# Optimization experiments

Hardware: AMD Instinct MI355X
Metric: run time of the kernel (lower is better)

## Reference

```python
import jax, jax.numpy as jnp
import numpy as np


def setup_inputs() -> dict:
    key = jax.random.key(0)
    ks = jax.random.split(key, 16)
    B, D, H = 65536, 64, 512
    s = 0.05
    inp = {
        "state": jax.random.normal(ks[0], (B, D), dtype=jnp.float32),
        "Wz0": jax.random.normal(ks[1], (H, D), dtype=jnp.float32) * s,
        "bz0": jax.random.normal(ks[2], (H,), dtype=jnp.float32) * s,
        "Wz1": jax.random.normal(ks[3], (H, H), dtype=jnp.float32) * s,
        "Wz2": jax.random.normal(ks[4], (H, H), dtype=jnp.float32) * s,
        "Wz3": jax.random.normal(ks[5], (H, H), dtype=jnp.float32) * s,
        "WzL": jax.random.normal(ks[6], (1, H), dtype=jnp.float32) * s,
        "Wx0": jax.random.normal(ks[7], (H, D), dtype=jnp.float32) * s,
        "bx0": jax.random.normal(ks[8], (H,), dtype=jnp.float32) * s,
        "Wx1": jax.random.normal(ks[9], (H, D), dtype=jnp.float32) * s,
        "bx1": jax.random.normal(ks[10], (H,), dtype=jnp.float32) * s,
        "Wx2": jax.random.normal(ks[11], (H, D), dtype=jnp.float32) * s,
        "bx2": jax.random.normal(ks[12], (H,), dtype=jnp.float32) * s,
        "WxL": jax.random.normal(ks[13], (1, D), dtype=jnp.float32) * s,
    }
    return inp


def reference(state, Wz0, bz0, Wz1, Wz2, Wz3, WzL, Wx0, bx0, Wx1, bx1, Wx2, bx2, WxL):
    sp = jax.nn.softplus

    def icnn_sum(x):  # x: [B, D] -> scalar (sum of per-sample convex outputs)
        z = sp(x @ Wz0.T + bz0)                      # [B, H]
        z = sp(z @ Wz1.T + x @ Wx0.T + bx0)          # [B, H]
        z = sp(z @ Wz2.T + x @ Wx1.T + bx1)          # [B, H]
        z = sp(z @ Wz3.T + x @ Wx2.T + bx2)          # [B, H]
        out = z @ WzL.T + x @ WxL.T                  # [B, 1]
        return out.sum()

    x = state - 1.0
    # Output is scalar per-sample, so grad of the batch-sum equals the stacked
    # per-sample jacobians computed by the torch Python loop.
    action = jax.grad(icnn_sum)(x)                   # [B, D]
    return action
```

## Files before the change

kernel.cpp:

```cpp
#include <hip/hip_runtime.h>

typedef unsigned short u16;
typedef unsigned int u32;
typedef unsigned long long u64;

#define B_TOTAL 65536
#define H 512
#define D 64
#define BM 64

typedef __bf16 bf16x8 __attribute__((ext_vector_type(8)));
typedef float f32x4 __attribute__((ext_vector_type(4)));

__device__ __forceinline__ u32 f2b(float f) {
  u32 u = __builtin_bit_cast(u32, f);
  return (u + 0x7fffu + ((u >> 16) & 1u)) >> 16;
}
__device__ __forceinline__ u16 f2bc(float f) {
  return __builtin_bit_cast(u16, (__bf16)f);
}
__device__ __forceinline__ float b2f(u32 bits) {
  return __builtin_bit_cast(float, bits << 16);
}

#define OFF_Wz0b 0
#define OFF_Wx0b 32768
#define OFF_Wx1b 65536
#define OFF_Wx2b 98304
#define OFF_Wz1b 131072
#define OFF_Wz2b 393216
#define OFF_Wz3b 655360
#define OFF_Wz1t 917504
#define OFF_Wz2t 1179648
#define OFF_Wz3t 1441792
#define OFF_Wz0t 1703936
#define OFF_Wx0t 1736704
#define OFF_Wx1t 1769472
#define OFF_Wx2t 1802240
#define OFF_WEND 1835008
#define WS_ELEMS OFF_WEND

__global__ __launch_bounds__(256) void prep_kernel(
    const float* __restrict__ Wz0, const float* __restrict__ Wz1,
    const float* __restrict__ Wz2, const float* __restrict__ Wz3,
    const float* __restrict__ Wx0, const float* __restrict__ Wx1,
    const float* __restrict__ Wx2, u16* __restrict__ wsb) {
  int i = blockIdx.x * 256 + threadIdx.x;
  const float* src;
  int NN, KK, trans, p;
  if (i < 131072) {
    int r = i >> 15; p = i & 32767;
    src = (r == 0) ? Wz0 : (r == 1) ? Wx0 : (r == 2) ? Wx1 : Wx2;
    NN = 512; KK = 64; trans = 0;
  } else if (i < 917504) {
    int j = i - 131072; int r = j >> 18; p = j & 262143;
    src = (r == 0) ? Wz1 : (r == 1) ? Wz2 : Wz3;
    NN = 512; KK = 512; trans = 0;
  } else if (i < 1703936) {
    int j = i - 917504; int r = j >> 18; p = j & 262143;
    src = (r == 0) ? Wz1 : (r == 1) ? Wz2 : Wz3;
    NN = 512; KK = 512; trans = 1;
  } else {
    int j = i - 1703936; int r = j >> 15; p = j & 32767;
    src = (r == 0) ? Wz0 : (r == 1) ? Wx0 : (r == 2) ? Wx1 : Wx2;
    NN = 64; KK = 512; trans = 1;
  }
  int jj = p & 7, lane = (p >> 3) & 63, blk = p >> 9;
  int kt_sh = (KK == 64) ? 1 : 4;
  int ntile = blk >> kt_sh;
  int kstep = blk & ((1 << kt_sh) - 1);
  int n = ntile * 16 + (lane & 15);
  int k = kstep * 32 + ((lane >> 4) << 3) + jj;
  float v = trans ? src[k * NN + n] : src[n * KK + k];
  wsb[i] = (u16)f2b(v);
}

__global__ __launch_bounds__(256) void fill_sentinel(float* out, int n) {
  int i = blockIdx.x * 256 + threadIdx.x;
  if (i < n) out[i] = 12345.0f;
}

__global__ __launch_bounds__(1024, 4) void icnn_kernel(
    const float* __restrict__ state,
    const float* __restrict__ bz0, const float* __restrict__ bx0,
    const float* __restrict__ bx1, const float* __restrict__ bx2,
    const float* __restrict__ WzL, const float* __restrict__ WxL,
    u16* __restrict__ wsw, float* __restrict__ out) {
  __shared__ u16 zbA[BM * H];
  __shared__ u16 zbB[BM * H];
  __shared__ u16 xbuf[BM * 72];

  const int tid = threadIdx.x;
  const int w = tid >> 6;
  const int lane = tid & 63;
  const int l15 = lane & 15;
  const int q = lane >> 4;
  const int blk = blockIdx.x;

  const u16* Wz0b = wsw + OFF_Wz0b;
  const u16* Wx0b = wsw + OFF_Wx0b;
  const u16* Wx1b = wsw + OFF_Wx1b;
  const u16* Wx2b = wsw + OFF_Wx2b;
  const u16* Wz1b = wsw + OFF_Wz1b;
  const u16* Wz2b = wsw + OFF_Wz2b;
  const u16* Wz3b = wsw + OFF_Wz3b;
  const u16* Wz1t = wsw + OFF_Wz1t;
  const u16* Wz2t = wsw + OFF_Wz2t;
  const u16* Wz3t = wsw + OFF_Wz3t;
  const u16* Wz0t = wsw + OFF_Wz0t;
  const u16* Wx0t = wsw + OFF_Wx0t;
  const u16* Wx1t = wsw + OFF_Wx1t;
  const u16* Wx2t = wsw + OFF_Wx2t;

  auto lbar = [&]() {
    asm volatile("s_waitcnt lgkmcnt(0)" ::: "memory");
    __builtin_amdgcn_s_barrier();
    asm volatile("" ::: "memory");
  };

  {
    int r = tid >> 4, c0 = (tid & 15) << 2;
    const float* p = state + (blk * BM + r) * D + c0;
    f32x4 v = __builtin_nontemporal_load((const f32x4*)p);
    u32* dst = (u32*)&xbuf[r * 72 + c0];
    dst[0] = (u32)f2bc(v[0] - 1.0f) | ((u32)f2bc(v[1] - 1.0f) << 16);
    dst[1] = (u32)f2bc(v[2] - 1.0f) | ((u32)f2bc(v[3] - 1.0f) << 16);
  }

  f32x4 acc[4][2];
  const f32x4 Z = {0.f, 0.f, 0.f, 0.f};
  f32x4 pk = Z;
  u64 sg0[8], sg1[8], sg2[8];

  auto ldA = [&](const u16* zb, int mt, int step) -> bf16x8 {
    return *(const bf16x8*)(&zb[(step * 4 + mt) * 512 + q * 128 + l15 * 8]);
  };
  auto ldX = [&](int mt, int ks) -> bf16x8 {
    return *(const bf16x8*)(&xbuf[(mt * 16 + l15) * 72 + ks * 32 + q * 8]);
  };
  auto wrZ = [&](u16* zb, int row, int n, u16 bits) {
    zb[((n >> 5) * 4 + (row >> 4)) * 512 + ((n >> 3) & 3) * 128 +
       (row & 15) * 8 + (n & 7)] = bits;
  };
  auto zeroAcc = [&]() {
#pragma unroll
    for (int mt = 0; mt < 4; ++mt)
#pragma unroll
      for (int nt = 0; nt < 2; ++nt) acc[mt][nt] = Z;
  };

  auto fwdX = [&](const u16* Wxp) {
    const u16* xb = Wxp + lane * 8;
#pragma unroll
    for (int ks = 0; ks < 2; ++ks) {
      bf16x8 b2[2];
#pragma unroll
      for (int nt = 0; nt < 2; ++nt)
        b2[nt] = *(const bf16x8*)(xb + ((w * 2 + nt) * 2 + ks) * 512);
#pragma unroll
      for (int mt = 0; mt < 4; ++mt) {
        bf16x8 ax = ldX(mt, ks);
#pragma unroll
        for (int nt = 0; nt < 2; ++nt) {
          f32x4 c = (ks == 0) ? Z : acc[mt][nt];
          acc[mt][nt] = __builtin_amdgcn_mfma_f32_16x16x32_bf16(ax, b2[nt], c, 0, 0, 0);
        }
      }
    }
  };

  auto fwdH = [&](const u16* Wp, const u16* zb) {
    const u16* gb = Wp + (w * 2 * 16) * 512 + lane * 8;
    bf16x8 b00 = *(const bf16x8*)(gb);
    bf16x8 b01 = *(const bf16x8*)(gb + 16 * 512);
    bf16x8 b10 = *(const bf16x8*)(gb + 512);
    bf16x8 b11 = *(const bf16x8*)(gb + 17 * 512);
#pragma unroll 2
    for (int st = 0; st < 16; ++st) {
      int stp = (st < 14) ? st + 2 : st;
      bf16x8 bn0 = *(const bf16x8*)(gb + stp * 512);
      bf16x8 bn1 = *(const bf16x8*)(gb + (16 + stp) * 512);
      bf16x8 a[4];
#pragma unroll
      for (int mt = 0; mt < 4; ++mt) a[mt] = ldA(zb, mt, st);
      __builtin_amdgcn_s_setprio(1);
#pragma unroll
      for (int mt = 0; mt < 4; ++mt)
        acc[mt][0] = __builtin_amdgcn_mfma_f32_16x16x32_bf16(
            a[mt], b00, acc[mt][0], 0, 0, 0);
#pragma unroll
      for (int mt = 0; mt < 4; ++mt)
        acc[mt][1] = __builtin_amdgcn_mfma_f32_16x16x32_bf16(
            a[mt], b01, acc[mt][1], 0, 0, 0);
      __builtin_amdgcn_s_setprio(0);
      b00 = b10; b01 = b11; b10 = bn0; b11 = bn1;
    }
  };

  auto fwd_epi = [&](const float* biasp, u64 (&sg)[8], u16* zb) {
    float bias[2];
#pragma unroll
    for (int nt = 0; nt < 2; ++nt) bias[nt] = biasp[(w * 2 + nt) * 16 + l15];
#pragma unroll
    for (int mt = 0; mt < 4; ++mt)
#pragma unroll
      for (int nt = 0; nt < 2; ++nt) {
        int n = (w * 2 + nt) * 16 + l15;
        f32x4 A = acc[mt][nt];
        u64 pack = 0;
#pragma unroll
        for (int r = 0; r < 4; ++r) {
          float a = A[r] + bias[nt];
          float t = __expf(-a);
          float u = 1.0f + t;
          float s = __builtin_amdgcn_rcpf(u);
          float z = a + __logf(u);
          pack |= (u64)f2bc(s) << (16 * r);
          wrZ(zb, mt * 16 + q * 4 + r, n, f2bc(z));
        }
        sg[mt * 2 + nt] = pack;
      }
  };
  auto d3_epi = [&](const float* biasp, u16* zb) {
    float bias[2], wl[2];
#pragma unroll
    for (int nt = 0; nt < 2; ++nt) {
      bias[nt] = biasp[(w * 2 + nt) * 16 + l15];
      wl[nt] = WzL[(w * 2 + nt) * 16 + l15];
    }
#pragma unroll
    for (int mt = 0; mt < 4; ++mt)
#pragma unroll
      for (int nt = 0; nt < 2; ++nt) {
        int n = (w * 2 + nt) * 16 + l15;
        f32x4 A = acc[mt][nt];
#pragma unroll
        for (int r = 0; r < 4; ++r) {
          float a = A[r] + bias[nt];
          float t = __expf(-a);
          float s = __builtin_amdgcn_rcpf(1.0f + t);
          wrZ(zb, mt * 16 + q * 4 + r, n, f2bc(wl[nt] * s));
        }
      }
  };
  auto bwd_epi = [&](const u64 (&sg)[8], u16* zb) {
#pragma unroll
    for (int mt = 0; mt < 4; ++mt)
#pragma unroll
      for (int nt = 0; nt < 2; ++nt) {
        int n = (w * 2 + nt) * 16 + l15;
        f32x4 A = acc[mt][nt];
        u64 v = sg[mt * 2 + nt];
#pragma unroll
        for (int r = 0; r < 4; ++r) {
          float s = b2f((u32)(v >> (16 * r)) & 0xffffu);
          wrZ(zb, mt * 16 + q * 4 + r, n, f2bc(A[r] * s));
        }
      }
  };

  auto minigrad = [&](const u16* Wg, const u16* zb, bool init) {
    int rt = w & 3, ct = w >> 2;
    const u16* gb = Wg + lane * 8;
    f32x4 ta = init ? Z : pk, tb = Z;
#pragma unroll 2
    for (int st = 0; st < 16; st += 2) {
      bf16x8 a0 = ldA(zb, rt, st);
      bf16x8 g0 = *(const bf16x8*)(gb + (ct * 16 + st) * 512);
      bf16x8 a1 = ldA(zb, rt, st + 1);
      bf16x8 g1 = *(const bf16x8*)(gb + (ct * 16 + st + 1) * 512);
      __builtin_amdgcn_s_setprio(1);
      ta = __builtin_amdgcn_mfma_f32_16x16x32_bf16(a0, g0, ta, 0, 0, 0);
      tb = __builtin_amdgcn_mfma_f32_16x16x32_bf16(a1, g1, tb, 0, 0, 0);
      __builtin_amdgcn_s_setprio(0);
    }
    pk = ta + tb;
  };

  lbar();
  fwdX(Wz0b);
  fwd_epi(bz0, sg0, zbA);
  lbar();
  fwdX(Wx0b); fwdH(Wz1b, zbA);
  fwd_epi(bx0, sg1, zbB);
  lbar();
  fwdX(Wx1b); fwdH(Wz2b, zbB);
  fwd_epi(bx1, sg2, zbA);
  lbar();
  fwdX(Wx2b); fwdH(Wz3b, zbA);
  d3_epi(bx2, zbB);
  lbar();
  minigrad(Wx2t, zbB, true);
  zeroAcc(); fwdH(Wz3t, zbB);
  bwd_epi(sg2, zbA);
  lbar();
  minigrad(Wx1t, zbA, false);
  zeroAcc(); fwdH(Wz2t, zbA);
  bwd_epi(sg1, zbB);
  lbar();
  minigrad(Wx0t, zbB, false);
  zeroAcc(); fwdH(Wz1t, zbB);
  bwd_epi(sg0, zbA);
  lbar();
  minigrad(Wz0t, zbA, false);
  {
    int rt = w & 3, ct = w >> 2;
    float wx = WxL[ct * 16 + l15];
#pragma unroll
    for (int r = 0; r < 4; ++r) {
      int row = blk * BM + rt * 16 + q * 4 + r;
      out[row * D + ct * 16 + l15] = pk[r] + wx;
    }
  }
}

extern "C" void kernel_launch(void* const* d_in, const int* in_sizes, int n_in,
                              void* d_out, int out_size, void* d_ws, size_t ws_size,
                              hipStream_t stream) {
  const float* state = (const float*)d_in[0];
  const float* Wz0 = (const float*)d_in[1];
  const float* bz0 = (const float*)d_in[2];
  const float* Wz1 = (const float*)d_in[3];
  const float* Wz2 = (const float*)d_in[4];
  const float* Wz3 = (const float*)d_in[5];
  const float* WzL = (const float*)d_in[6];
  const float* Wx0 = (const float*)d_in[7];
  const float* bx0 = (const float*)d_in[8];
  const float* Wx1 = (const float*)d_in[9];
  const float* bx1 = (const float*)d_in[10];
  const float* Wx2 = (const float*)d_in[11];
  const float* bx2 = (const float*)d_in[12];
  const float* WxL = (const float*)d_in[13];

  if (ws_size < (size_t)WS_ELEMS * 2) {
    fill_sentinel<<<(out_size + 255) / 256, 256, 0, stream>>>((float*)d_out, out_size);
    return;
  }
  u16* wsw = (u16*)d_ws;
  prep_kernel<<<OFF_WEND / 256, 256, 0, stream>>>(Wz0, Wz1, Wz2, Wz3, Wx0, Wx1, Wx2, wsw);
  icnn_kernel<<<B_TOTAL / BM, 1024, 0, stream>>>(state, bz0, bx0, bx1, bx2, WzL, WxL,
                                                 wsw, (float*)d_out);
}
```

Baseline: 406.7 us.

## Halve batch tile to 32 rows with 8 waves each owning 64 columns

Shrinks the per-block batch tile from 64 to 32 rows and the block from 16 to 8 waves. Each wave now covers 4 column tiles by 2 row tiles instead of 2 by 4, so every weight fragment it loads feeds fewer MFMAs. The weight prefetch distance drops from two steps to one. LDS use per block halves, which should let more blocks reside per CU, but global/L2 weight traffic per sample doubles.

```diff
diff --git a/kernel.cpp b/kernel.cpp
--- a/kernel.cpp
+++ b/kernel.cpp
@@ -7,7 +7,7 @@
 #define B_TOTAL 65536
 #define H 512
 #define D 64
-#define BM 64
+#define BM 32
 
 typedef __bf16 bf16x8 __attribute__((ext_vector_type(8)));
 typedef float f32x4 __attribute__((ext_vector_type(4)));
@@ -80,7 +80,7 @@
   if (i < n) out[i] = 12345.0f;
 }
 
-__global__ __launch_bounds__(1024, 4) void icnn_kernel(
+__global__ __launch_bounds__(512, 4) void icnn_kernel(
     const float* __restrict__ state,
     const float* __restrict__ bz0, const float* __restrict__ bx0,
     const float* __restrict__ bx1, const float* __restrict__ bx2,
@@ -127,85 +127,91 @@
     dst[1] = (u32)f2bc(v[2] - 1.0f) | ((u32)f2bc(v[3] - 1.0f) << 16);
   }
 
-  f32x4 acc[4][2];
+  f32x4 acc[2][4];
   const f32x4 Z = {0.f, 0.f, 0.f, 0.f};
   f32x4 pk = Z;
   u64 sg0[8], sg1[8], sg2[8];
 
   auto ldA = [&](const u16* zb, int mt, int step) -> bf16x8 {
-    return *(const bf16x8*)(&zb[(step * 4 + mt) * 512 + q * 128 + l15 * 8]);
+    return *(const bf16x8*)(&zb[(step * 2 + mt) * 512 + q * 128 + l15 * 8]);
   };
   auto ldX = [&](int mt, int ks) -> bf16x8 {
     return *(const bf16x8*)(&xbuf[(mt * 16 + l15) * 72 + ks * 32 + q * 8]);
   };
   auto wrZ = [&](u16* zb, int row, int n, u16 bits) {
-    zb[((n >> 5) * 4 + (row >> 4)) * 512 + ((n >> 3) & 3) * 128 +
+    zb[((n >> 5) * 2 + (row >> 4)) * 512 + ((n >> 3) & 3) * 128 +
        (row & 15) * 8 + (n & 7)] = bits;
   };
   auto zeroAcc = [&]() {
 #pragma unroll
-    for (int mt = 0; mt < 4; ++mt)
-#pragma unroll
-      for (int nt = 0; nt < 2; ++nt) acc[mt][nt] = Z;
+    for (int mt = 0; mt < 2; ++mt)
+#pragma unroll
+      for (int nt = 0; nt < 4; ++nt) acc[mt][nt] = Z;
   };
 
   auto fwdX = [&](const u16* Wxp) {
     const u16* xb = Wxp + lane * 8;
 #pragma unroll
     for (int ks = 0; ks < 2; ++ks) {
-      bf16x8 b2[2];
-#pragma unroll
-      for (int nt = 0; nt < 2; ++nt)
-        b2[nt] = *(const bf16x8*)(xb + ((w * 2 + nt) * 2 + ks) * 512);
-#pragma unroll
-      for (int mt = 0; mt < 4; ++mt) {
+      bf16x8 b4[4];
+#pragma unroll
+      for (int nt = 0; nt < 4; ++nt)
+        b4[nt] = *(const bf16x8*)(xb + ((w * 4 + nt) * 2 + ks) * 512);
+#pragma unroll
+      for (int mt = 0; mt < 2; ++mt) {
         bf16x8 ax = ldX(mt, ks);
 #pragma unroll
-        for (int nt = 0; nt < 2; ++nt) {
+        for (int nt = 0; nt < 4; ++nt) {
           f32x4 c = (ks == 0) ? Z : acc[mt][nt];
-          acc[mt][nt] = __builtin_amdgcn_mfma_f32_16x16x32_bf16(ax, b2[nt], c, 0, 0, 0);
+          acc[mt][nt] = __builtin_amdgcn_mfma_f32_16x16x32_bf16(ax, b4[nt], c, 0, 0, 0);
         }
       }
     }
   };
 
   auto fwdH = [&](const u16* Wp, const u16* zb) {
-    const u16* gb = Wp + (w * 2 * 16) * 512 + lane * 8;
-    bf16x8 b00 = *(const bf16x8*)(gb);
-    bf16x8 b01 = *(const bf16x8*)(gb + 16 * 512);
-    bf16x8 b10 = *(const bf16x8*)(gb + 512);
-    bf16x8 b11 = *(const bf16x8*)(gb + 17 * 512);
+    const u16* gb = Wp + (w * 4 * 16) * 512 + lane * 8;
+    bf16x8 bc0 = *(const bf16x8*)(gb);
+    bf16x8 bc1 = *(const bf16x8*)(gb + 16 * 512);
+    bf16x8 bc2 = *(const bf16x8*)(gb + 32 * 512);
+    bf16x8 bc3 = *(const bf16x8*)(gb + 48 * 512);
 #pragma unroll 2
     for (int st = 0; st < 16; ++st) {
-      int stp = (st < 14) ? st + 2 : st;
-      bf16x8 bn0 = *(const bf16x8*)(gb + stp * 512);
-      bf16x8 bn1 = *(const bf16x8*)(gb + (16 + stp) * 512);
-      bf16x8 a[4];
-#pragma unroll
-      for (int mt = 0; mt < 4; ++mt) a[mt] = ldA(zb, mt, st);
+      int stn = (st < 15) ? st + 1 : st;
+      bf16x8 bn0 = *(const bf16x8*)(gb + stn * 512);
+      bf16x8 bn1 = *(const bf16x8*)(gb + (16 + stn) * 512);
+      bf16x8 bn2 = *(const bf16x8*)(gb + (32 + stn) * 512);
+      bf16x8 bn3 = *(const bf16x8*)(gb + (48 + stn) * 512);
+      bf16x8 a[2];
+#pragma unroll
+      for (int mt = 0; mt < 2; ++mt) a[mt] = ldA(zb, mt, st);
       __builtin_amdgcn_s_setprio(1);
 #pragma unroll
-      for (int mt = 0; mt < 4; ++mt)
-        acc[mt][0] = __builtin_amdgcn_mfma_f32_16x16x32_bf16(
-            a[mt], b00, acc[mt][0], 0, 0, 0);
-#pragma unroll
-      for (int mt = 0; mt < 4; ++mt)
-        acc[mt][1] = __builtin_amdgcn_mfma_f32_16x16x32_bf16(
-            a[mt], b01, acc[mt][1], 0, 0, 0);
+      for (int mt = 0; mt < 2; ++mt)
+        acc[mt][0] = __builtin_amdgcn_mfma_f32_16x16x32_bf16(a[mt], bc0, acc[mt][0], 0, 0, 0);
+#pragma unroll
+      for (int mt = 0; mt < 2; ++mt)
+        acc[mt][1] = __builtin_amdgcn_mfma_f32_16x16x32_bf16(a[mt], bc1, acc[mt][1], 0, 0, 0);
+#pragma unroll
+      for (int mt = 0; mt < 2; ++mt)
+        acc[mt][2] = __builtin_amdgcn_mfma_f32_16x16x32_bf16(a[mt], bc2, acc[mt][2], 0, 0, 0);
+#pragma unroll
+      for (int mt = 0; mt < 2; ++mt)
+        acc[mt][3] = __builtin_amdgcn_mfma_f32_16x16x32_bf16(a[mt], bc3, acc[mt][3], 0, 0, 0);
       __builtin_amdgcn_s_setprio(0);
-      b00 = b10; b01 = b11; b10 = bn0; b11 = bn1;
+      bc0 = bn0; bc1 = bn1; bc2 = bn2; bc3 = bn3;
     }
   };
 
   auto fwd_epi = [&](const float* biasp, u64 (&sg)[8], u16* zb) {
-    float bias[2];
-#pragma unroll
-    for (int nt = 0; nt < 2; ++nt) bias[nt] = biasp[(w * 2 + nt) * 16 + l15];
-#pragma unroll
-    for (int mt = 0; mt < 4; ++mt)
-#pragma unroll
-      for (int nt = 0; nt < 2; ++nt) {
-        int n = (w * 2 + nt) * 16 + l15;
+    float bias[4];
+#pragma unroll
+    for (int nt = 0; nt < 4; ++nt) bias[nt] = biasp[(w * 4 + nt) * 16 + l15];
+#pragma unroll
+    for (int mt = 0; mt < 2; ++mt)
+#pragma unroll
+      for (int nt = 0; nt < 4; ++nt) {
+        int n = (w * 4 + nt) * 16 + l15;
         f32x4 A = acc[mt][nt];
         u64 pack = 0;
 #pragma unroll
@@ -218,21 +224,21 @@
           pack |= (u64)f2bc(s) << (16 * r);
           wrZ(zb, mt * 16 + q * 4 + r, n, f2bc(z));
         }
-        sg[mt * 2 + nt] = pack;
+        sg[mt * 4 + nt] = pack;
       }
   };
   auto d3_epi = [&](const float* biasp, u16* zb) {
-    float bias[2], wl[2];
-#pragma unroll
-    for (int nt = 0; nt < 2; ++nt) {
-      bias[nt] = biasp[(w * 2 + nt) * 16 + l15];
-      wl[nt] = WzL[(w * 2 + nt) * 16 + l15];
-    }
-#pragma unroll
-    for (int mt = 0; mt < 4; ++mt)
-#pragma unroll
-      for (int nt = 0; nt < 2; ++nt) {
-        int n = (w * 2 + nt) * 16 + l15;
+    float bias[4], wl[4];
+#pragma unroll
+    for (int nt = 0; nt < 4; ++nt) {
+      bias[nt] = biasp[(w * 4 + nt) * 16 + l15];
+      wl[nt] = WzL[(w * 4 + nt) * 16 + l15];
+    }
+#pragma unroll
+    for (int mt = 0; mt < 2; ++mt)
+#pragma unroll
+      for (int nt = 0; nt < 4; ++nt) {
+        int n = (w * 4 + nt) * 16 + l15;
         f32x4 A = acc[mt][nt];
 #pragma unroll
         for (int r = 0; r < 4; ++r) {
@@ -245,12 +251,12 @@
   };
   auto bwd_epi = [&](const u64 (&sg)[8], u16* zb) {
 #pragma unroll
-    for (int mt = 0; mt < 4; ++mt)
-#pragma unroll
-      for (int nt = 0; nt < 2; ++nt) {
-        int n = (w * 2 + nt) * 16 + l15;
+    for (int mt = 0; mt < 2; ++mt)
+#pragma unroll
+      for (int nt = 0; nt < 4; ++nt) {
+        int n = (w * 4 + nt) * 16 + l15;
         f32x4 A = acc[mt][nt];
-        u64 v = sg[mt * 2 + nt];
+        u64 v = sg[mt * 4 + nt];
 #pragma unroll
         for (int r = 0; r < 4; ++r) {
           float s = b2f((u32)(v >> (16 * r)) & 0xffffu);
@@ -260,7 +266,7 @@
   };
 
   auto minigrad = [&](const u16* Wg, const u16* zb, bool init) {
-    int rt = w & 3, ct = w >> 2;
+    int rt = w & 1, ct = w >> 1;
     const u16* gb = Wg + lane * 8;
     f32x4 ta = init ? Z : pk, tb = Z;
 #pragma unroll 2
@@ -304,7 +310,7 @@
   lbar();
   minigrad(Wz0t, zbA, false);
   {
-    int rt = w & 3, ct = w >> 2;
+    int rt = w & 1, ct = w >> 1;
     float wx = WxL[ct * 16 + l15];
 #pragma unroll
     for (int r = 0; r < 4; ++r) {
@@ -338,6 +344,6 @@
   }
   u16* wsw = (u16*)d_ws;
   prep_kernel<<<OFF_WEND / 256, 256, 0, stream>>>(Wz0, Wz1, Wz2, Wz3, Wx0, Wx1, Wx2, wsw);
-  icnn_kernel<<<B_TOTAL / BM, 1024, 0, stream>>>(state, bz0, bx0, bx1, bx2, WzL, WxL,
-                                                 wsw, (float*)d_out);
-}
+  icnn_kernel<<<B_TOTAL / BM, 512, 0, stream>>>(state, bz0, bx0, bx1, bx2, WzL, WxL,
+                                                wsw, (float*)d_out);
+}
```

Result: slower. 454.1 us (+11.7%).
